# Kernel optimization log

Measured on AMD Instinct MI355X. Metric: run time of the kernel, lower is better.

Reference implementation:

```python
import jax, jax.numpy as jnp
import numpy as np

B, T, HW, ENC, DEC, ATT, EMB, V = 32, 128, 14, 2048, 512, 512, 512, 10000
P = HW * HW  # num_pixels = 196


def setup_inputs() -> dict:
    key = jax.random.key(0)
    ks = jax.random.split(key, 24)
    s = 0.02
    inp = {
        'bimgs': jax.random.normal(ks[0], (B, HW, HW, ENC), dtype=jnp.float32),
        'bx': jax.random.randint(ks[1], (B, T), 0, V),
        # torch code assumes lengths sorted DESCENDING
        'bxlen': jnp.sort(jax.random.randint(ks[2], (B,), 1, T + 1))[::-1],
        'emb_W': jax.random.normal(ks[3], (V, EMB)) * s,
        'enc_att_W': jax.random.normal(ks[4], (ATT, ENC)) * s,
        'enc_att_b': jnp.zeros((ATT,)),
        'dec_att_W': jax.random.normal(ks[5], (ATT, DEC)) * s,
        'dec_att_b': jnp.zeros((ATT,)),
        'full_att_W': jax.random.normal(ks[6], (1, ATT)) * s,
        'full_att_b': jnp.zeros((1,)),
        'init_h_W': jax.random.normal(ks[7], (DEC, ENC)) * s,
        'init_h_b': jnp.zeros((DEC,)),
        'init_c_W': jax.random.normal(ks[8], (DEC, ENC)) * s,
        'init_c_b': jnp.zeros((DEC,)),
        'f_beta_W': jax.random.normal(ks[9], (ENC, DEC)) * s,
        'f_beta_b': jnp.zeros((ENC,)),
        'W_ih': jax.random.normal(ks[10], (4 * DEC, EMB + ENC)) * s,
        'b_ih': jnp.zeros((4 * DEC,)),
        'W_hh': jax.random.normal(ks[11], (4 * DEC, DEC)) * s,
        'b_hh': jnp.zeros((4 * DEC,)),
        'fc_W': jax.random.normal(ks[12], (V, DEC)) * s,
        'fc_b': jnp.zeros((V,)),
    }
    return inp


def reference(bimgs, bx, bxlen, emb_W, enc_att_W, enc_att_b, dec_att_W, dec_att_b,
              full_att_W, full_att_b, init_h_W, init_h_b, init_c_W, init_c_b,
              f_beta_W, f_beta_b, W_ih, b_ih, W_hh, b_hh, fc_W, fc_b):
    b = bimgs.shape[0]
    imgs = bimgs.reshape(b, -1, bimgs.shape[-1])          # [B,P,enc]
    t_len = bx.shape[-1]
    embeds = emb_W[bx]                                     # [B,T,E]
    mean_img = imgs.mean(axis=1)                           # [B,enc]
    h0 = mean_img @ init_h_W.T + init_h_b                  # [B,dec]
    c0 = mean_img @ init_c_W.T + init_c_b
    # encoder attention projection is time-invariant -> hoist out of the loop
    att1 = imgs @ enc_att_W.T + enc_att_b                  # [B,P,A]
    active_ts = jnp.arange(t_len)[:, None] < bxlen[None, :]  # [T,B]
    emb_ts = embeds.transpose(1, 0, 2)                     # [T,B,E]

    def step(carry, xs):
        h, c = carry
        emb_t, active = xs
        att2 = h @ dec_att_W.T + dec_att_b                 # [B,A]
        e = jax.nn.relu(att1 + att2[:, None, :]) @ full_att_W[0] + full_att_b[0]  # [B,P]
        alpha = jax.nn.softmax(e, axis=1)
        awe = jnp.einsum('bpe,bp->be', imgs, alpha)        # [B,enc]
        gate = jax.nn.sigmoid(h @ f_beta_W.T + f_beta_b)
        x = jnp.concatenate([emb_t, gate * awe], axis=1)   # [B,E+enc]
        # PyTorch LSTMCell: gate order i, f, g, o
        gates = x @ W_ih.T + b_ih + h @ W_hh.T + b_hh
        i_, f_, g_, o_ = jnp.split(gates, 4, axis=1)
        i_ = jax.nn.sigmoid(i_); f_ = jax.nn.sigmoid(f_); o_ = jax.nn.sigmoid(o_)
        g_ = jnp.tanh(g_)
        c_new = f_ * c + i_ * g_
        h_new = o_ * jnp.tanh(c_new)
        preds = h_new @ fc_W.T + fc_b                      # dropout = identity (eval)
        m = active[:, None]
        h2 = jnp.where(m, h_new, h)
        c2 = jnp.where(m, c_new, c)
        return (h2, c2), (jnp.where(m, preds, 0.0), jnp.where(m, alpha, 0.0))

    _, (preds_ts, alphas_ts) = jax.lax.scan(step, (h0, c0), (emb_ts, active_ts))
    predictions = preds_ts.transpose(1, 0, 2)              # [B,T,V]
    alphas = alphas_ts.transpose(1, 0, 2)                  # [B,T,P]
    return predictions, alphas
```

## Files before the change

kernel.cpp:

```cpp
#include <hip/hip_runtime.h>
#include <hip/hip_bf16.h>

#define BB 32
#define TT 128
#define PP 196
#define ENC 2048
#define DEC 512
#define ATT 512
#define EMB 512
#define VV 10000
#define G4 2048
#define KX 2560

typedef unsigned short u16;
typedef unsigned int u32;
typedef __attribute__((ext_vector_type(8))) short short8;
typedef __attribute__((ext_vector_type(4))) float f32x4;

__device__ __forceinline__ float bf2f(u16 u) { return __uint_as_float(((u32)u) << 16); }
__device__ __forceinline__ u16 f2bf(float f) {
  u32 x = __float_as_uint(f);
  u32 r = (x + 0x7fffu + ((x >> 16) & 1u)) >> 16;
  return (u16)r;
}
__device__ __forceinline__ void unpack8(uint4 v, float* f) {
  f[0] = __uint_as_float(v.x << 16); f[1] = __uint_as_float(v.x & 0xffff0000u);
  f[2] = __uint_as_float(v.y << 16); f[3] = __uint_as_float(v.y & 0xffff0000u);
  f[4] = __uint_as_float(v.z << 16); f[5] = __uint_as_float(v.z & 0xffff0000u);
  f[6] = __uint_as_float(v.w << 16); f[7] = __uint_as_float(v.w & 0xffff0000u);
}
__device__ __forceinline__ void load8(const float* __restrict__ p, float* f) {
  float4 a = ((const float4*)p)[0];
  float4 b = ((const float4*)p)[1];
  f[0] = a.x; f[1] = a.y; f[2] = a.z; f[3] = a.w;
  f[4] = b.x; f[5] = b.y; f[6] = b.z; f[7] = b.w;
}
__device__ __forceinline__ float sigf(float x) { return 1.0f / (1.0f + __expf(-x)); }
__device__ __forceinline__ short8 ld_frag(const u16* __restrict__ p) {
  union { uint4 u; short8 s; } cv;
  cv.u = *(const uint4*)p;
  return cv.s;
}

__global__ __launch_bounds__(256) void k_cvt(const float* __restrict__ src, u16* __restrict__ dst, int n) {
  int i0 = (blockIdx.x * 256 + threadIdx.x) * 8;
  if (i0 >= n) return;
  float f[8]; load8(src + i0, f);
  u16 o[8];
#pragma unroll
  for (int u = 0; u < 8; u++) o[u] = f2bf(f[u]);
  *(uint4*)(dst + i0) = *(const uint4*)o;
}

__global__ __launch_bounds__(256) void k_init(const float* __restrict__ imgs,
    const float* __restrict__ ihW, const float* __restrict__ ihb,
    const float* __restrict__ icW, const float* __restrict__ icb,
    u16* __restrict__ h_bf, float* __restrict__ c) {
  __shared__ float mean_s[ENC];
  int b = blockIdx.x, tid = threadIdx.x;
  for (int i = 0; i < ENC / 256; i++) {
    int ch = tid + i * 256;
    float s = 0.f;
    for (int p = 0; p < PP; p++) s += imgs[(size_t)(b * PP + p) * ENC + ch];
    mean_s[ch] = s * (1.0f / PP);
  }
  __syncthreads();
  for (int i = 0; i < 4; i++) {
    int o = tid + i * 256;
    int j = o & 511; int which = o >> 9;
    const float* W = which ? icW : ihW;
    const float* bias = which ? icb : ihb;
    const float* wr = W + (size_t)j * ENC;
    float acc = 0.f;
    for (int k = 0; k < ENC; k += 8) {
      float wf[8]; load8(wr + k, wf);
#pragma unroll
      for (int u = 0; u < 8; u++) acc += wf[u] * mean_s[k + u];
    }
    acc += bias[j];
    if (which) c[b * DEC + j] = acc; else h_bf[b * DEC + j] = f2bf(acc);
  }
}

__global__ __launch_bounds__(512) void k_att1(const float* __restrict__ imgs,
    const float* __restrict__ W, const float* __restrict__ bias, u16* __restrict__ att1) {
  __shared__ float a_s[8 * ENC];
  int m0 = blockIdx.x * 8, tid = threadIdx.x;
  for (int i = 0; i < (8 * ENC) / 512; i++) {
    int flat = i * 512 + tid;
    int m = flat >> 11, k = flat & 2047;
    a_s[k * 8 + m] = imgs[(size_t)(m0 + m) * ENC + k];
  }
  __syncthreads();
  int j = tid;
  const float* wr = W + (size_t)j * ENC;
  float acc[8] = {0,0,0,0,0,0,0,0};
  for (int k = 0; k < ENC; k += 8) {
    float wf[8]; load8(wr + k, wf);
#pragma unroll
    for (int u = 0; u < 8; u++) {
      const float4* ap = (const float4*)&a_s[(k + u) * 8];
      float4 a0 = ap[0], a1 = ap[1];
      acc[0] += wf[u] * a0.x; acc[1] += wf[u] * a0.y;
      acc[2] += wf[u] * a0.z; acc[3] += wf[u] * a0.w;
      acc[4] += wf[u] * a1.x; acc[5] += wf[u] * a1.y;
      acc[6] += wf[u] * a1.z; acc[7] += wf[u] * a1.w;
    }
  }
  float bj = bias[j];
#pragma unroll
  for (int m = 0; m < 8; m++)
    att1[(size_t)(m0 + m) * ATT + j] = f2bf(acc[m] + bj);
}

__global__ __launch_bounds__(64) void k_step1(const u16* __restrict__ W3,
    const float* __restrict__ decb, const float* __restrict__ fbb, const float* __restrict__ bhh,
    const u16* __restrict__ h_bf,
    float* __restrict__ att2, float* __restrict__ gate, float* __restrict__ hWhh) {
  int lane = threadIdx.x;
  int j0 = blockIdx.x * 16;
  int m = lane & 15, quad = lane >> 4;
  const u16* arow = W3 + (size_t)(j0 + m) * DEC + quad * 8;
  const u16* xb0 = h_bf + (size_t)m * DEC + quad * 8;
  const u16* xb1 = h_bf + (size_t)(16 + m) * DEC + quad * 8;
  f32x4 acc0 = {0.f,0.f,0.f,0.f}, acc1 = {0.f,0.f,0.f,0.f};
  for (int k = 0; k < DEC; k += 32) {
    short8 a = ld_frag(arow + k);
    short8 x0 = ld_frag(xb0 + k);
    short8 x1 = ld_frag(xb1 + k);
    acc0 = __builtin_amdgcn_mfma_f32_16x16x32_bf16(a, x0, acc0, 0, 0, 0);
    acc1 = __builtin_amdgcn_mfma_f32_16x16x32_bf16(a, x1, acc1, 0, 0, 0);
  }
  int jj = j0 + quad * 4;
  int b0 = m, b1 = 16 + m;
#pragma unroll
  for (int r = 0; r < 4; r++) {
    int j = jj + r;
    float v0 = acc0[r], v1 = acc1[r];
    if (j0 < ATT) {
      float bia = decb[j];
      att2[b0 * ATT + j] = v0 + bia;
      att2[b1 * ATT + j] = v1 + bia;
    } else if (j0 < ATT + ENC) {
      int g = j - ATT;
      float bia = fbb[g];
      gate[b0 * ENC + g] = sigf(v0 + bia);
      gate[b1 * ENC + g] = sigf(v1 + bia);
    } else {
      int g = j - ATT - ENC;
      float bia = bhh[g];
      hWhh[b0 * G4 + g] = v0 + bia;
      hWhh[b1 * G4 + g] = v1 + bia;
    }
  }
}

__global__ __launch_bounds__(256) void k_att(int t, const int* __restrict__ bxlen,
    const u16* __restrict__ att1, const float* __restrict__ att2,
    const float* __restrict__ faW, const float* __restrict__ fab,
    float* __restrict__ alpha_ws, float* __restrict__ out_alphas) {
  int b = blockIdx.x;
  if (t >= bxlen[b]) return;
  __shared__ float a2[ATT];
  __shared__ float w_s[ATT];
  __shared__ float red[256];
  int tid = threadIdx.x;
  for (int i = tid; i < ATT; i += 256) { a2[i] = att2[b * ATT + i]; w_s[i] = faW[i]; }
  __syncthreads();
  float e = -1e30f;
  if (tid < PP) {
    const uint4* ar = (const uint4*)(att1 + (size_t)(b * PP + tid) * ATT);
    float acc = 0.f;
    for (int k = 0; k < ATT; k += 8) {
      float af[8]; unpack8(ar[k >> 3], af);
#pragma unroll
      for (int u = 0; u < 8; u++) {
        float v = af[u] + a2[k + u];
        acc += fmaxf(v, 0.f) * w_s[k + u];
      }
    }
    e = acc + fab[0];
  }
  red[tid] = e; __syncthreads();
  for (int s = 128; s > 0; s >>= 1) { if (tid < s) red[tid] = fmaxf(red[tid], red[tid + s]); __syncthreads(); }
  float mx = red[0]; __syncthreads();
  float ex = (tid < PP) ? __expf(e - mx) : 0.f;
  red[tid] = ex; __syncthreads();
  for (int s = 128; s > 0; s >>= 1) { if (tid < s) red[tid] += red[tid + s]; __syncthreads(); }
  float inv = 1.0f / red[0];
  if (tid < PP) {
    float al = ex * inv;
    alpha_ws[b * PP + tid] = al;
    out_alphas[((size_t)b * TT + t) * PP + tid] = al;
  }
}

__global__ __launch_bounds__(256) void k_awe(int t, const int* __restrict__ bxlen,
    const int* __restrict__ bx, const float* __restrict__ embW,
    const u16* __restrict__ imgs_bf, const float* __restrict__ alpha_ws,
    const float* __restrict__ gate, u16* __restrict__ x_bf) {
  int b = blockIdx.x / 9, chunk = blockIdx.x % 9;
  if (t >= bxlen[b]) return;
  int tid = threadIdx.x;
  if (chunk == 8) {
    int tok = bx[b * TT + t];
    int ch = tid * 2;
    x_bf[b * KX + ch]     = f2bf(embW[(size_t)tok * EMB + ch]);
    x_bf[b * KX + ch + 1] = f2bf(embW[(size_t)tok * EMB + ch + 1]);
    return;
  }
  __shared__ float al[PP];
  if (tid < PP) al[tid] = alpha_ws[b * PP + tid];
  __syncthreads();
  int ch = chunk * 256 + tid;
  float acc = 0.f;
  for (int p = 0; p < PP; p++)
    acc += al[p] * bf2f(imgs_bf[(size_t)(b * PP + p) * ENC + ch]);
  x_bf[b * KX + EMB + ch] = f2bf(gate[b * ENC + ch] * acc);
}

__global__ __launch_bounds__(64) void k_gates(const u16* __restrict__ Wih_bf,
    const u16* __restrict__ x_bf, float* __restrict__ gates_p) {
  int lane = threadIdx.x;
  int j0 = blockIdx.x * 16;
  int kc = blockIdx.y * 640;
  int m = lane & 15, quad = lane >> 4;
  const u16* arow = Wih_bf + (size_t)(j0 + m) * KX + kc + quad * 8;
  const u16* xb0 = x_bf + (size_t)m * KX + kc + quad * 8;
  const u16* xb1 = x_bf + (size_t)(16 + m) * KX + kc + quad * 8;
  f32x4 acc0 = {0.f,0.f,0.f,0.f}, acc1 = {0.f,0.f,0.f,0.f};
  for (int k = 0; k < 640; k += 32) {
    short8 a = ld_frag(arow + k);
    short8 x0 = ld_frag(xb0 + k);
    short8 x1 = ld_frag(xb1 + k);
    acc0 = __builtin_amdgcn_mfma_f32_16x16x32_bf16(a, x0, acc0, 0, 0, 0);
    acc1 = __builtin_amdgcn_mfma_f32_16x16x32_bf16(a, x1, acc1, 0, 0, 0);
  }
  float* gp = gates_p + (size_t)blockIdx.y * BB * G4;
  int jj = j0 + quad * 4;
  int b0 = m, b1 = 16 + m;
#pragma unroll
  for (int r = 0; r < 4; r++) {
    int j = jj + r;
    gp[b0 * G4 + j] = acc0[r];
    gp[b1 * G4 + j] = acc1[r];
  }
}

__global__ __launch_bounds__(256) void k_lstm(int t, const int* __restrict__ bxlen,
    const float* __restrict__ gates_p, const float* __restrict__ bih,
    const float* __restrict__ hWhh,
    u16* __restrict__ h_bf, float* __restrict__ c) {
  int idx = blockIdx.x * 256 + threadIdx.x;
  int b = idx >> 9, d = idx & 511;
  if (t >= bxlen[b]) return;
  float pre[4];
#pragma unroll
  for (int g = 0; g < 4; g++) {
    int j = g * 512 + d;
    float s = bih[j] + hWhh[b * G4 + j];
#pragma unroll
    for (int cc = 0; cc < 4; cc++) s += gates_p[(size_t)cc * BB * G4 + b * G4 + j];
    pre[g] = s;
  }
  float i_ = sigf(pre[0]);
  float f_ = sigf(pre[1]);
  float g_ = tanhf(pre[2]);
  float o_ = sigf(pre[3]);
  float cn = f_ * c[b * DEC + d] + i_ * g_;
  float hn = o_ * tanhf(cn);
  c[b * DEC + d] = cn;
  h_bf[b * DEC + d] = f2bf(hn);
}

__global__ __launch_bounds__(64) void k_fc(int t, const int* __restrict__ bxlen,
    const u16* __restrict__ fcW_bf, const float* __restrict__ fcb,
    const u16* __restrict__ h_bf, float* __restrict__ preds) {
  int lane = threadIdx.x;
  int j0 = blockIdx.x * 16;
  int m = lane & 15, quad = lane >> 4;
  const u16* arow = fcW_bf + (size_t)(j0 + m) * DEC + quad * 8;
  const u16* xb0 = h_bf + (size_t)m * DEC + quad * 8;
  const u16* xb1 = h_bf + (size_t)(16 + m) * DEC + quad * 8;
  f32x4 acc0 = {0.f,0.f,0.f,0.f}, acc1 = {0.f,0.f,0.f,0.f};
  for (int k = 0; k < DEC; k += 32) {
    short8 a = ld_frag(arow + k);
    short8 x0 = ld_frag(xb0 + k);
    short8 x1 = ld_frag(xb1 + k);
    acc0 = __builtin_amdgcn_mfma_f32_16x16x32_bf16(a, x0, acc0, 0, 0, 0);
    acc1 = __builtin_amdgcn_mfma_f32_16x16x32_bf16(a, x1, acc1, 0, 0, 0);
  }
  int jj = j0 + quad * 4;
  int b0 = m, b1 = 16 + m;
  bool act0 = (t < bxlen[b0]);
  bool act1 = (t < bxlen[b1]);
#pragma unroll
  for (int r = 0; r < 4; r++) {
    int j = jj + r;
    float bia = fcb[j];
    if (act0) preds[((size_t)b0 * TT + t) * VV + j] = acc0[r] + bia;
    if (act1) preds[((size_t)b1 * TT + t) * VV + j] = acc1[r] + bia;
  }
}

extern "C" void kernel_launch(void* const* d_in, const int* in_sizes, int n_in,
                              void* d_out, int out_size, void* d_ws, size_t ws_size,
                              hipStream_t stream) {
  const float* imgs = (const float*)d_in[0];
  const int* bx     = (const int*)d_in[1];
  const int* bxlen  = (const int*)d_in[2];
  const float* embW = (const float*)d_in[3];
  const float* encW = (const float*)d_in[4];
  const float* encb = (const float*)d_in[5];
  const float* decW = (const float*)d_in[6];
  const float* decb = (const float*)d_in[7];
  const float* faW  = (const float*)d_in[8];
  const float* fab  = (const float*)d_in[9];
  const float* ihW  = (const float*)d_in[10];
  const float* ihb  = (const float*)d_in[11];
  const float* icW  = (const float*)d_in[12];
  const float* icb  = (const float*)d_in[13];
  const float* fbW  = (const float*)d_in[14];
  const float* fbb  = (const float*)d_in[15];
  const float* Wih  = (const float*)d_in[16];
  const float* bih  = (const float*)d_in[17];
  const float* Whh  = (const float*)d_in[18];
  const float* bhh  = (const float*)d_in[19];
  const float* fcW  = (const float*)d_in[20];
  const float* fcb  = (const float*)d_in[21];

  float* out_preds  = (float*)d_out;
  float* out_alphas = out_preds + (size_t)BB * TT * VV;

  char* wsb = (char*)d_ws;
  size_t off = 0;
  u16* imgs_bf = (u16*)(wsb + off); off += (size_t)BB * PP * ENC * 2;
  u16* W3_bf   = (u16*)(wsb + off); off += (size_t)4608 * DEC * 2;
  u16* Wih_bf  = (u16*)(wsb + off); off += (size_t)G4 * KX * 2;
  u16* fcW_bf  = (u16*)(wsb + off); off += (size_t)VV * DEC * 2;
  u16* att1    = (u16*)(wsb + off); off += (size_t)BB * PP * ATT * 2;
  u16* x_bf    = (u16*)(wsb + off); off += (size_t)BB * KX * 2;
  u16* h_bf    = (u16*)(wsb + off); off += (size_t)BB * DEC * 2;
  float* c      = (float*)(wsb + off); off += (size_t)BB * DEC * 4;
  float* att2   = (float*)(wsb + off); off += (size_t)BB * ATT * 4;
  float* gate   = (float*)(wsb + off); off += (size_t)BB * ENC * 4;
  float* hWhh   = (float*)(wsb + off); off += (size_t)BB * G4 * 4;
  float* gates_p = (float*)(wsb + off); off += (size_t)4 * BB * G4 * 4;
  float* alpha  = (float*)(wsb + off); off += (size_t)BB * PP * 4;

  hipMemsetAsync(d_out, 0, (size_t)out_size * sizeof(float), stream);

  k_cvt<<<(BB * PP * ENC) / 2048, 256, 0, stream>>>(imgs, imgs_bf, BB * PP * ENC);
  k_cvt<<<(DEC * DEC) / 2048, 256, 0, stream>>>(decW, W3_bf, DEC * DEC);
  k_cvt<<<(ENC * DEC) / 2048, 256, 0, stream>>>(fbW, W3_bf + (size_t)DEC * DEC, ENC * DEC);
  k_cvt<<<(G4 * DEC) / 2048, 256, 0, stream>>>(Whh, W3_bf + (size_t)(DEC + ENC) * DEC, G4 * DEC);
  k_cvt<<<(G4 * KX) / 2048, 256, 0, stream>>>(Wih, Wih_bf, G4 * KX);
  k_cvt<<<(VV * DEC) / 2048, 256, 0, stream>>>(fcW, fcW_bf, VV * DEC);

  k_init<<<BB, 256, 0, stream>>>(imgs, ihW, ihb, icW, icb, h_bf, c);
  k_att1<<<(BB * PP) / 8, 512, 0, stream>>>(imgs, encW, encb, att1);

  for (int t = 0; t < TT; t++) {
    k_step1<<<4608 / 16, 64, 0, stream>>>(W3_bf, decb, fbb, bhh, h_bf, att2, gate, hWhh);
    k_att<<<BB, 256, 0, stream>>>(t, bxlen, att1, att2, faW, fab, alpha, out_alphas);
    k_awe<<<BB * 9, 256, 0, stream>>>(t, bxlen, bx, embW, imgs_bf, alpha, gate, x_bf);
    k_gates<<<dim3(G4 / 16, 4), 64, 0, stream>>>(Wih_bf, x_bf, gates_p);
    k_lstm<<<(BB * DEC) / 256, 256, 0, stream>>>(t, bxlen, gates_p, bih, hWhh, h_bf, c);
    k_fc<<<VV / 16, 64, 0, stream>>>(t, bxlen, fcW_bf, fcb, h_bf, out_preds);
  }
}
```

Before: 7.248 ms.

## Fuse fc into next-step stage, MFMA precompute, drop output memset, shuffle softmax

Folds the fc projection of step t-1 and the embedding gather into a single combined stage-1 kernel, cutting per-step launches. The att1 and init projections are rewritten to use bf16 MFMA on pre-converted weights, and the mean is computed from bf16 images. The output memset is removed; predictions and alphas now write explicit zeros for inactive steps. Softmax reductions use wave shuffles and the awe kernel is vectorised. This trades some init precision for fewer launches and less redundant memory traffic.

Result: faster. 6.786 ms (-6.4%).

```diff
diff --git a/kernel.cpp b/kernel.cpp
--- a/kernel.cpp
+++ b/kernel.cpp
@@ -52,79 +52,33 @@
   *(uint4*)(dst + i0) = *(const uint4*)o;
 }
 
-__global__ __launch_bounds__(256) void k_init(const float* __restrict__ imgs,
-    const float* __restrict__ ihW, const float* __restrict__ ihb,
-    const float* __restrict__ icW, const float* __restrict__ icb,
-    u16* __restrict__ h_bf, float* __restrict__ c) {
-  __shared__ float mean_s[ENC];
-  int b = blockIdx.x, tid = threadIdx.x;
-  for (int i = 0; i < ENC / 256; i++) {
-    int ch = tid + i * 256;
-    float s = 0.f;
-    for (int p = 0; p < PP; p++) s += imgs[(size_t)(b * PP + p) * ENC + ch];
-    mean_s[ch] = s * (1.0f / PP);
-  }
-  __syncthreads();
-  for (int i = 0; i < 4; i++) {
-    int o = tid + i * 256;
-    int j = o & 511; int which = o >> 9;
-    const float* W = which ? icW : ihW;
-    const float* bias = which ? icb : ihb;
-    const float* wr = W + (size_t)j * ENC;
-    float acc = 0.f;
-    for (int k = 0; k < ENC; k += 8) {
-      float wf[8]; load8(wr + k, wf);
-#pragma unroll
-      for (int u = 0; u < 8; u++) acc += wf[u] * mean_s[k + u];
-    }
-    acc += bias[j];
-    if (which) c[b * DEC + j] = acc; else h_bf[b * DEC + j] = f2bf(acc);
-  }
-}
-
-__global__ __launch_bounds__(512) void k_att1(const float* __restrict__ imgs,
-    const float* __restrict__ W, const float* __restrict__ bias, u16* __restrict__ att1) {
-  __shared__ float a_s[8 * ENC];
-  int m0 = blockIdx.x * 8, tid = threadIdx.x;
-  for (int i = 0; i < (8 * ENC) / 512; i++) {
-    int flat = i * 512 + tid;
-    int m = flat >> 11, k = flat & 2047;
-    a_s[k * 8 + m] = imgs[(size_t)(m0 + m) * ENC + k];
-  }
-  __syncthreads();
-  int j = tid;
-  const float* wr = W + (size_t)j * ENC;
-  float acc[8] = {0,0,0,0,0,0,0,0};
-  for (int k = 0; k < ENC; k += 8) {
-    float wf[8]; load8(wr + k, wf);
-#pragma unroll
-    for (int u = 0; u < 8; u++) {
-      const float4* ap = (const float4*)&a_s[(k + u) * 8];
-      float4 a0 = ap[0], a1 = ap[1];
-      acc[0] += wf[u] * a0.x; acc[1] += wf[u] * a0.y;
-      acc[2] += wf[u] * a0.z; acc[3] += wf[u] * a0.w;
-      acc[4] += wf[u] * a1.x; acc[5] += wf[u] * a1.y;
-      acc[6] += wf[u] * a1.z; acc[7] += wf[u] * a1.w;
-    }
-  }
-  float bj = bias[j];
-#pragma unroll
-  for (int m = 0; m < 8; m++)
-    att1[(size_t)(m0 + m) * ATT + j] = f2bf(acc[m] + bj);
-}
-
-__global__ __launch_bounds__(64) void k_step1(const u16* __restrict__ W3,
-    const float* __restrict__ decb, const float* __restrict__ fbb, const float* __restrict__ bhh,
-    const u16* __restrict__ h_bf,
-    float* __restrict__ att2, float* __restrict__ gate, float* __restrict__ hWhh) {
+__global__ __launch_bounds__(256) void k_mean(const u16* __restrict__ imgs_bf, u16* __restrict__ mean_bf) {
+  int b = blockIdx.x >> 2, chunk = blockIdx.x & 3;
+  int ch0 = chunk * 512 + threadIdx.x * 2;
+  const u32* base = (const u32*)(imgs_bf + (size_t)b * PP * ENC + ch0);
+  float a0 = 0.f, a1 = 0.f;
+#pragma unroll 4
+  for (int p = 0; p < PP; p++) {
+    u32 u = base[(size_t)p * (ENC / 2)];
+    a0 += __uint_as_float(u << 16);
+    a1 += __uint_as_float(u & 0xffff0000u);
+  }
+  const float inv = 1.0f / PP;
+  u16 o[2] = { f2bf(a0 * inv), f2bf(a1 * inv) };
+  *(u32*)(mean_bf + b * ENC + ch0) = *(const u32*)o;
+}
+
+__global__ __launch_bounds__(64) void k_init2(const u16* __restrict__ W2_bf,
+    const float* __restrict__ ihb, const float* __restrict__ icb,
+    const u16* __restrict__ mean_bf, u16* __restrict__ h_bf, float* __restrict__ c) {
   int lane = threadIdx.x;
   int j0 = blockIdx.x * 16;
   int m = lane & 15, quad = lane >> 4;
-  const u16* arow = W3 + (size_t)(j0 + m) * DEC + quad * 8;
-  const u16* xb0 = h_bf + (size_t)m * DEC + quad * 8;
-  const u16* xb1 = h_bf + (size_t)(16 + m) * DEC + quad * 8;
+  const u16* arow = W2_bf + (size_t)(j0 + m) * ENC + quad * 8;
+  const u16* xb0 = mean_bf + (size_t)m * ENC + quad * 8;
+  const u16* xb1 = mean_bf + (size_t)(16 + m) * ENC + quad * 8;
   f32x4 acc0 = {0.f,0.f,0.f,0.f}, acc1 = {0.f,0.f,0.f,0.f};
-  for (int k = 0; k < DEC; k += 32) {
+  for (int k = 0; k < ENC; k += 32) {
     short8 a = ld_frag(arow + k);
     short8 x0 = ld_frag(xb0 + k);
     short8 x1 = ld_frag(xb1 + k);
@@ -136,22 +90,140 @@
 #pragma unroll
   for (int r = 0; r < 4; r++) {
     int j = jj + r;
-    float v0 = acc0[r], v1 = acc1[r];
-    if (j0 < ATT) {
-      float bia = decb[j];
-      att2[b0 * ATT + j] = v0 + bia;
-      att2[b1 * ATT + j] = v1 + bia;
-    } else if (j0 < ATT + ENC) {
-      int g = j - ATT;
-      float bia = fbb[g];
-      gate[b0 * ENC + g] = sigf(v0 + bia);
-      gate[b1 * ENC + g] = sigf(v1 + bia);
+    if (j < 512) {
+      float bia = ihb[j];
+      h_bf[b0 * DEC + j] = f2bf(acc0[r] + bia);
+      h_bf[b1 * DEC + j] = f2bf(acc1[r] + bia);
     } else {
-      int g = j - ATT - ENC;
-      float bia = bhh[g];
-      hWhh[b0 * G4 + g] = v0 + bia;
-      hWhh[b1 * G4 + g] = v1 + bia;
-    }
+      int g = j - 512;
+      float bia = icb[g];
+      c[b0 * DEC + g] = acc0[r] + bia;
+      c[b1 * DEC + g] = acc1[r] + bia;
+    }
+  }
+}
+
+__global__ __launch_bounds__(256) void k_att1(const u16* __restrict__ imgs_bf,
+    const u16* __restrict__ encW_bf, const float* __restrict__ encb, u16* __restrict__ att1) {
+  int tid = threadIdx.x;
+  int wave = tid >> 6, lane = tid & 63;
+  int m0 = blockIdx.x * 32;
+  int lm = lane & 15, quad = lane >> 4;
+  const u16* b0p = imgs_bf + (size_t)(m0 + lm) * ENC + quad * 8;
+  const u16* b1p = imgs_bf + (size_t)(m0 + 16 + lm) * ENC + quad * 8;
+  const u16* arow = encW_bf + (size_t)(wave * 128 + lm) * ENC + quad * 8;
+  f32x4 acc[8][2];
+#pragma unroll
+  for (int i = 0; i < 8; i++) { acc[i][0] = (f32x4){0.f,0.f,0.f,0.f}; acc[i][1] = (f32x4){0.f,0.f,0.f,0.f}; }
+  for (int k = 0; k < ENC; k += 32) {
+    short8 B0 = ld_frag(b0p + k);
+    short8 B1 = ld_frag(b1p + k);
+#pragma unroll
+    for (int i = 0; i < 8; i++) {
+      short8 A = ld_frag(arow + (size_t)i * 16 * ENC + k);
+      acc[i][0] = __builtin_amdgcn_mfma_f32_16x16x32_bf16(A, B0, acc[i][0], 0, 0, 0);
+      acc[i][1] = __builtin_amdgcn_mfma_f32_16x16x32_bf16(A, B1, acc[i][1], 0, 0, 0);
+    }
+  }
+#pragma unroll
+  for (int i = 0; i < 8; i++) {
+    int jb = wave * 128 + i * 16 + quad * 4;
+#pragma unroll
+    for (int r = 0; r < 4; r++) {
+      int j = jb + r;
+      float bia = encb[j];
+      att1[(size_t)(m0 + lm) * ATT + j]      = f2bf(acc[i][0][r] + bia);
+      att1[(size_t)(m0 + 16 + lm) * ATT + j] = f2bf(acc[i][1][r] + bia);
+    }
+  }
+}
+
+__global__ __launch_bounds__(64) void k_stage1(int t,
+    const int* __restrict__ bx, const int* __restrict__ bxlen,
+    const u16* __restrict__ W3, const float* __restrict__ decb,
+    const float* __restrict__ fbb, const float* __restrict__ bhh,
+    const u16* __restrict__ h_bf,
+    float* __restrict__ att2, float* __restrict__ gate, float* __restrict__ hWhh,
+    const u16* __restrict__ fcW_bf, const float* __restrict__ fcb, float* __restrict__ preds,
+    const float* __restrict__ embW, u16* __restrict__ x_bf) {
+  int bid = blockIdx.x;
+  int lane = threadIdx.x;
+  if (bid < 288) {
+    if (t >= TT) return;
+    int j0 = bid * 16;
+    int m = lane & 15, quad = lane >> 4;
+    const u16* arow = W3 + (size_t)(j0 + m) * DEC + quad * 8;
+    const u16* xb0 = h_bf + (size_t)m * DEC + quad * 8;
+    const u16* xb1 = h_bf + (size_t)(16 + m) * DEC + quad * 8;
+    f32x4 acc0 = {0.f,0.f,0.f,0.f}, acc1 = {0.f,0.f,0.f,0.f};
+    for (int k = 0; k < DEC; k += 32) {
+      short8 a = ld_frag(arow + k);
+      short8 x0 = ld_frag(xb0 + k);
+      short8 x1 = ld_frag(xb1 + k);
+      acc0 = __builtin_amdgcn_mfma_f32_16x16x32_bf16(a, x0, acc0, 0, 0, 0);
+      acc1 = __builtin_amdgcn_mfma_f32_16x16x32_bf16(a, x1, acc1, 0, 0, 0);
+    }
+    int jj = j0 + quad * 4;
+    int b0 = m, b1 = 16 + m;
+#pragma unroll
+    for (int r = 0; r < 4; r++) {
+      int j = jj + r;
+      float v0 = acc0[r], v1 = acc1[r];
+      if (j0 < ATT) {
+        float bia = decb[j];
+        att2[b0 * ATT + j] = v0 + bia;
+        att2[b1 * ATT + j] = v1 + bia;
+      } else if (j0 < ATT + ENC) {
+        int g = j - ATT;
+        float bia = fbb[g];
+        gate[b0 * ENC + g] = sigf(v0 + bia);
+        gate[b1 * ENC + g] = sigf(v1 + bia);
+      } else {
+        int g = j - ATT - ENC;
+        float bia = bhh[g];
+        hWhh[b0 * G4 + g] = v0 + bia;
+        hWhh[b1 * G4 + g] = v1 + bia;
+      }
+    }
+  } else if (bid < 913) {
+    if (t == 0) return;
+    int tfc = t - 1;
+    int j0 = (bid - 288) * 16;
+    int m = lane & 15, quad = lane >> 4;
+    const u16* arow = fcW_bf + (size_t)(j0 + m) * DEC + quad * 8;
+    const u16* xb0 = h_bf + (size_t)m * DEC + quad * 8;
+    const u16* xb1 = h_bf + (size_t)(16 + m) * DEC + quad * 8;
+    f32x4 acc0 = {0.f,0.f,0.f,0.f}, acc1 = {0.f,0.f,0.f,0.f};
+    for (int k = 0; k < DEC; k += 32) {
+      short8 a = ld_frag(arow + k);
+      short8 x0 = ld_frag(xb0 + k);
+      short8 x1 = ld_frag(xb1 + k);
+      acc0 = __builtin_amdgcn_mfma_f32_16x16x32_bf16(a, x0, acc0, 0, 0, 0);
+      acc1 = __builtin_amdgcn_mfma_f32_16x16x32_bf16(a, x1, acc1, 0, 0, 0);
+    }
+    int jj = j0 + quad * 4;
+    int b0 = m, b1 = 16 + m;
+    bool act0 = (tfc < bxlen[b0]);
+    bool act1 = (tfc < bxlen[b1]);
+#pragma unroll
+    for (int r = 0; r < 4; r++) {
+      int j = jj + r;
+      float bia = fcb[j];
+      preds[((size_t)b0 * TT + tfc) * VV + j] = act0 ? (acc0[r] + bia) : 0.f;
+      preds[((size_t)b1 * TT + tfc) * VV + j] = act1 ? (acc1[r] + bia) : 0.f;
+    }
+  } else {
+    if (t >= TT) return;
+    int flat = (bid - 913) * 64 + lane;
+    int b = flat >> 5;
+    int ch0 = (flat & 31) * 16;
+    int tok = bx[b * TT + t];
+    const float* e = embW + (size_t)tok * EMB + ch0;
+    u16 o[16];
+#pragma unroll
+    for (int u = 0; u < 16; u++) o[u] = f2bf(e[u]);
+    *(uint4*)(x_bf + (size_t)b * KX + ch0)     = *(const uint4*)o;
+    *(uint4*)(x_bf + (size_t)b * KX + ch0 + 8) = *(const uint4*)(o + 8);
   }
 }
 
@@ -160,11 +232,14 @@
     const float* __restrict__ faW, const float* __restrict__ fab,
     float* __restrict__ alpha_ws, float* __restrict__ out_alphas) {
   int b = blockIdx.x;
-  if (t >= bxlen[b]) return;
+  int tid = threadIdx.x;
+  if (t >= bxlen[b]) {
+    if (tid < PP) out_alphas[((size_t)b * TT + t) * PP + tid] = 0.f;
+    return;
+  }
   __shared__ float a2[ATT];
   __shared__ float w_s[ATT];
-  __shared__ float red[256];
-  int tid = threadIdx.x;
+  __shared__ float redw[4], redw2[4];
   for (int i = tid; i < ATT; i += 256) { a2[i] = att2[b * ATT + i]; w_s[i] = faW[i]; }
   __syncthreads();
   float e = -1e30f;
@@ -181,13 +256,20 @@
     }
     e = acc + fab[0];
   }
-  red[tid] = e; __syncthreads();
-  for (int s = 128; s > 0; s >>= 1) { if (tid < s) red[tid] = fmaxf(red[tid], red[tid + s]); __syncthreads(); }
-  float mx = red[0]; __syncthreads();
+  int lane = tid & 63, wid = tid >> 6;
+  float wmax = e;
+#pragma unroll
+  for (int off = 32; off; off >>= 1) wmax = fmaxf(wmax, __shfl_xor(wmax, off));
+  if (lane == 0) redw[wid] = wmax;
+  __syncthreads();
+  float mx = fmaxf(fmaxf(redw[0], redw[1]), fmaxf(redw[2], redw[3]));
   float ex = (tid < PP) ? __expf(e - mx) : 0.f;
-  red[tid] = ex; __syncthreads();
-  for (int s = 128; s > 0; s >>= 1) { if (tid < s) red[tid] += red[tid + s]; __syncthreads(); }
-  float inv = 1.0f / red[0];
+  float wsum = ex;
+#pragma unroll
+  for (int off = 32; off; off >>= 1) wsum += __shfl_xor(wsum, off);
+  if (lane == 0) redw2[wid] = wsum;
+  __syncthreads();
+  float inv = 1.0f / (redw2[0] + redw2[1] + redw2[2] + redw2[3]);
   if (tid < PP) {
     float al = ex * inv;
     alpha_ws[b * PP + tid] = al;
@@ -196,27 +278,27 @@
 }
 
 __global__ __launch_bounds__(256) void k_awe(int t, const int* __restrict__ bxlen,
-    const int* __restrict__ bx, const float* __restrict__ embW,
     const u16* __restrict__ imgs_bf, const float* __restrict__ alpha_ws,
     const float* __restrict__ gate, u16* __restrict__ x_bf) {
-  int b = blockIdx.x / 9, chunk = blockIdx.x % 9;
+  int b = blockIdx.x >> 2, chunk = blockIdx.x & 3;
   if (t >= bxlen[b]) return;
+  __shared__ float al[PP];
   int tid = threadIdx.x;
-  if (chunk == 8) {
-    int tok = bx[b * TT + t];
-    int ch = tid * 2;
-    x_bf[b * KX + ch]     = f2bf(embW[(size_t)tok * EMB + ch]);
-    x_bf[b * KX + ch + 1] = f2bf(embW[(size_t)tok * EMB + ch + 1]);
-    return;
-  }
-  __shared__ float al[PP];
   if (tid < PP) al[tid] = alpha_ws[b * PP + tid];
   __syncthreads();
-  int ch = chunk * 256 + tid;
-  float acc = 0.f;
-  for (int p = 0; p < PP; p++)
-    acc += al[p] * bf2f(imgs_bf[(size_t)(b * PP + p) * ENC + ch]);
-  x_bf[b * KX + EMB + ch] = f2bf(gate[b * ENC + ch] * acc);
+  int ch0 = chunk * 512 + tid * 2;
+  const u32* base = (const u32*)(imgs_bf + (size_t)b * PP * ENC + ch0);
+  float acc0 = 0.f, acc1 = 0.f;
+#pragma unroll 4
+  for (int p = 0; p < PP; p++) {
+    u32 u = base[(size_t)p * (ENC / 2)];
+    float a = al[p];
+    acc0 += a * __uint_as_float(u << 16);
+    acc1 += a * __uint_as_float(u & 0xffff0000u);
+  }
+  float2 g = *(const float2*)(gate + b * ENC + ch0);
+  u16 o[2] = { f2bf(g.x * acc0), f2bf(g.y * acc1) };
+  *(u32*)(x_bf + (size_t)b * KX + EMB + ch0) = *(const u32*)o;
 }
 
 __global__ __launch_bounds__(64) void k_gates(const u16* __restrict__ Wih_bf,
@@ -271,36 +353,6 @@
   float hn = o_ * tanhf(cn);
   c[b * DEC + d] = cn;
   h_bf[b * DEC + d] = f2bf(hn);
-}
-
-__global__ __launch_bounds__(64) void k_fc(int t, const int* __restrict__ bxlen,
-    const u16* __restrict__ fcW_bf, const float* __restrict__ fcb,
-    const u16* __restrict__ h_bf, float* __restrict__ preds) {
-  int lane = threadIdx.x;
-  int j0 = blockIdx.x * 16;
-  int m = lane & 15, quad = lane >> 4;
-  const u16* arow = fcW_bf + (size_t)(j0 + m) * DEC + quad * 8;
-  const u16* xb0 = h_bf + (size_t)m * DEC + quad * 8;
-  const u16* xb1 = h_bf + (size_t)(16 + m) * DEC + quad * 8;
-  f32x4 acc0 = {0.f,0.f,0.f,0.f}, acc1 = {0.f,0.f,0.f,0.f};
-  for (int k = 0; k < DEC; k += 32) {
-    short8 a = ld_frag(arow + k);
-    short8 x0 = ld_frag(xb0 + k);
-    short8 x1 = ld_frag(xb1 + k);
-    acc0 = __builtin_amdgcn_mfma_f32_16x16x32_bf16(a, x0, acc0, 0, 0, 0);
-    acc1 = __builtin_amdgcn_mfma_f32_16x16x32_bf16(a, x1, acc1, 0, 0, 0);
-  }
-  int jj = j0 + quad * 4;
-  int b0 = m, b1 = 16 + m;
-  bool act0 = (t < bxlen[b0]);
-  bool act1 = (t < bxlen[b1]);
-#pragma unroll
-  for (int r = 0; r < 4; r++) {
-    int j = jj + r;
-    float bia = fcb[j];
-    if (act0) preds[((size_t)b0 * TT + t) * VV + j] = acc0[r] + bia;
-    if (act1) preds[((size_t)b1 * TT + t) * VV + j] = acc1[r] + bia;
-  }
 }
 
 extern "C" void kernel_launch(void* const* d_in, const int* in_sizes, int n_in,
@@ -338,7 +390,11 @@
   u16* W3_bf   = (u16*)(wsb + off); off += (size_t)4608 * DEC * 2;
   u16* Wih_bf  = (u16*)(wsb + off); off += (size_t)G4 * KX * 2;
   u16* fcW_bf  = (u16*)(wsb + off); off += (size_t)VV * DEC * 2;
-  u16* att1    = (u16*)(wsb + off); off += (size_t)BB * PP * ATT * 2;
+  u16* encW_bf = (u16*)(wsb + off); off += (size_t)ATT * ENC * 2;
+  u16* att1    = (u16*)(wsb + off);
+  u16* W2_bf   = att1;
+  u16* mean_bf = att1 + (size_t)1024 * ENC;
+  off += (size_t)BB * PP * ATT * 2;
   u16* x_bf    = (u16*)(wsb + off); off += (size_t)BB * KX * 2;
   u16* h_bf    = (u16*)(wsb + off); off += (size_t)BB * DEC * 2;
   float* c      = (float*)(wsb + off); off += (size_t)BB * DEC * 4;
@@ -348,24 +404,28 @@
   float* gates_p = (float*)(wsb + off); off += (size_t)4 * BB * G4 * 4;
   float* alpha  = (float*)(wsb + off); off += (size_t)BB * PP * 4;
 
-  hipMemsetAsync(d_out, 0, (size_t)out_size * sizeof(float), stream);
-
   k_cvt<<<(BB * PP * ENC) / 2048, 256, 0, stream>>>(imgs, imgs_bf, BB * PP * ENC);
   k_cvt<<<(DEC * DEC) / 2048, 256, 0, stream>>>(decW, W3_bf, DEC * DEC);
   k_cvt<<<(ENC * DEC) / 2048, 256, 0, stream>>>(fbW, W3_bf + (size_t)DEC * DEC, ENC * DEC);
   k_cvt<<<(G4 * DEC) / 2048, 256, 0, stream>>>(Whh, W3_bf + (size_t)(DEC + ENC) * DEC, G4 * DEC);
   k_cvt<<<(G4 * KX) / 2048, 256, 0, stream>>>(Wih, Wih_bf, G4 * KX);
   k_cvt<<<(VV * DEC) / 2048, 256, 0, stream>>>(fcW, fcW_bf, VV * DEC);
-
-  k_init<<<BB, 256, 0, stream>>>(imgs, ihW, ihb, icW, icb, h_bf, c);
-  k_att1<<<(BB * PP) / 8, 512, 0, stream>>>(imgs, encW, encb, att1);
+  k_cvt<<<(ATT * ENC) / 2048, 256, 0, stream>>>(encW, encW_bf, ATT * ENC);
+  k_cvt<<<(DEC * ENC) / 2048, 256, 0, stream>>>(ihW, W2_bf, DEC * ENC);
+  k_cvt<<<(DEC * ENC) / 2048, 256, 0, stream>>>(icW, W2_bf + (size_t)DEC * ENC, DEC * ENC);
+
+  k_mean<<<BB * 4, 256, 0, stream>>>(imgs_bf, mean_bf);
+  k_init2<<<64, 64, 0, stream>>>(W2_bf, ihb, icb, mean_bf, h_bf, c);
+  k_att1<<<(BB * PP) / 32, 256, 0, stream>>>(imgs_bf, encW_bf, encb, att1);
 
   for (int t = 0; t < TT; t++) {
-    k_step1<<<4608 / 16, 64, 0, stream>>>(W3_bf, decb, fbb, bhh, h_bf, att2, gate, hWhh);
+    k_stage1<<<929, 64, 0, stream>>>(t, bx, bxlen, W3_bf, decb, fbb, bhh, h_bf,
+                                     att2, gate, hWhh, fcW_bf, fcb, out_preds, embW, x_bf);
     k_att<<<BB, 256, 0, stream>>>(t, bxlen, att1, att2, faW, fab, alpha, out_alphas);
-    k_awe<<<BB * 9, 256, 0, stream>>>(t, bxlen, bx, embW, imgs_bf, alpha, gate, x_bf);
+    k_awe<<<BB * 4, 256, 0, stream>>>(t, bxlen, imgs_bf, alpha, gate, x_bf);
     k_gates<<<dim3(G4 / 16, 4), 64, 0, stream>>>(Wih_bf, x_bf, gates_p);
     k_lstm<<<(BB * DEC) / 256, 256, 0, stream>>>(t, bxlen, gates_p, bih, hWhh, h_bf, c);
-    k_fc<<<VV / 16, 64, 0, stream>>>(t, bxlen, fcW_bf, fcb, h_bf, out_preds);
-  }
-}
+  }
+  k_stage1<<<929, 64, 0, stream>>>(TT, bx, bxlen, W3_bf, decb, fbb, bhh, h_bf,
+                                   att2, gate, hWhh, fcW_bf, fcb, out_preds, embW, x_bf);
+}
```
